# Performance work log

Measured on AMD Instinct MI355X. Metric: run time of the kernel, lower is better.

The kernel has to match this reference:

```python
import jax, jax.numpy as jnp
import numpy as np

KERNEL_SIZE = 16
STRIDE = 8
NEG = -1.0e9


def setup_inputs() -> dict:
    key = jax.random.key(0)
    k1, k2, k3, k4, k5 = jax.random.split(key, 5)
    B, C, L = 8, 512, 4096
    x = jax.random.normal(k1, (B, C, L), dtype=jnp.float32)
    mask = jax.random.randint(k2, (B, L), 0, 2).astype(bool)
    W = jax.random.normal(k3, (C, C), dtype=jnp.float32) * 0.02
    b = jax.random.normal(k4, (C,), dtype=jnp.float32) * 0.02
    v = jax.random.normal(k5, (C,), dtype=jnp.float32) * 0.02
    return {"x": x, "mask": mask, "W": W, "b": b, "v": v}


def reference(x, mask, W, b, v):
    # x: [B, C, L], mask: [B, L] (True = masked out)
    B, C, L = x.shape
    win, step = KERNEL_SIZE, STRIDE
    L_pool = 1 + (L - win) // step
    # per-token projection (identical across windows since proj is per-token)
    h = jnp.tanh(jnp.einsum('bcl,dc->bld', x, W) + b)      # [B, L, C]
    s = jnp.einsum('bld,d->bl', h, v)                       # [B, L]
    idx = jnp.arange(L_pool)[:, None] * step + jnp.arange(win)[None, :]
    sw = s[:, idx]
    mw = mask[:, idx]
    sw = jnp.where(mw, NEG, sw)
    w = jax.nn.softmax(sw, axis=-1)
    w = jnp.where(mw, 0.0, w)
    norm = jnp.clip(jnp.sum(w, axis=-1, keepdims=True), 1e-6, None)
    w = w / norm
    xw = x[:, :, idx]
    return jnp.einsum('bcpw,bpw->bcp', xw, w)               # [B, C, L_pool]
```

## Files before the change

kernel.cpp:

```cpp
#include <hip/hip_runtime.h>
#include <hip/hip_bf16.h>
#include <cmath>

#define Bsz 8
#define Csz 512
#define Lsz 4096
#define LPOOL 511
#define NEGV -1000000000.0f

typedef __attribute__((ext_vector_type(8))) short short8;
typedef __attribute__((ext_vector_type(4))) float float4v;

__device__ __forceinline__ float bf2f(short u) {
  unsigned int x = ((unsigned int)(unsigned short)u) << 16;
  return __builtin_bit_cast(float, x);
}

__device__ __forceinline__ void gl_lds16(const __hip_bfloat16* g, void* l) {
  __builtin_amdgcn_global_load_lds(
      (const __attribute__((address_space(1))) unsigned int*)g,
      (__attribute__((address_space(3))) unsigned int*)l, 16, 0, 0);
}

__global__ __launch_bounds__(256) void stage1(const float* __restrict__ x,
    __hip_bfloat16* __restrict__ xTs, __hip_bfloat16* __restrict__ xbf,
    const unsigned char* __restrict__ mb, int* __restrict__ flag,
    const float* __restrict__ W, __hip_bfloat16* __restrict__ Wts) {
  const int tid = threadIdx.x;
  const int bid = blockIdx.x;
  if (bid < 4096) {
    __shared__ float sX[64][65];
    const int lt = bid & 63, ct = (bid >> 6) & 7, b = bid >> 9;
    const int l0 = lt * 64;
    const float* xb = x + ((size_t)b * Csz + ct * 64) * Lsz + l0;
    #pragma unroll
    for (int it = 0; it < 4; ++it) {
      int c = it * 16 + (tid >> 4);
      int l = (tid & 15) * 4;
      *(float4*)(&sX[c][l]) = *(const float4*)(xb + (size_t)c * Lsz + l);
    }
    __syncthreads();
    #pragma unroll
    for (int it = 0; it < 2; ++it) {
      int u = it * 256 + tid;
      int cg = u >> 6, ll = u & 63;
      __hip_bfloat16 hb[8];
      #pragma unroll
      for (int j = 0; j < 8; ++j)
        hb[j] = __float2bfloat16(sX[cg * 8 + j][ll]);
      int m = b * Lsz + l0 + ll;
      int mt = m >> 7, row = m & 127;
      int cglob = ct * 64 + cg * 8;
      int ks = cglob >> 5, seg = (cglob >> 3) & 3;
      *(short8*)(xTs + (((size_t)mt * 16 + ks) * 512 + seg * 128 + row) * 8) = *(short8*)hb;
    }
    #pragma unroll
    for (int it = 0; it < 2; ++it) {
      int u = it * 256 + tid;
      int cg = u >> 3, lseg = u & 7;
      __hip_bfloat16 hb[8];
      #pragma unroll
      for (int j = 0; j < 8; ++j)
        hb[j] = __float2bfloat16(sX[cg][lseg * 8 + j]);
      *(short8*)(xbf + ((size_t)b * Csz + ct * 64 + cg) * Lsz + l0 + lseg * 8) = *(short8*)hb;
    }
  } else {
    const int pb = bid - 4096;
    if (pb == 0) {
      __shared__ int sf;
      if (tid == 0) sf = 0;
      __syncthreads();
      int f = 0;
      for (int i = tid; i < 4096; i += 256)
        if ((i & 3) && mb[i]) f = 1;
      if (f) atomicOr(&sf, 1);
      __syncthreads();
      if (tid == 0) *flag = sf;
    } else {
      int tg = (pb - 1) * 256 + tid;
      int d = tg >> 6, cg = tg & 63;
      float4 w0 = *(const float4*)(W + (size_t)d * 512 + cg * 8);
      float4 w1 = *(const float4*)(W + (size_t)d * 512 + cg * 8 + 4);
      __hip_bfloat16 hb[8];
      hb[0] = __float2bfloat16(w0.x); hb[1] = __float2bfloat16(w0.y);
      hb[2] = __float2bfloat16(w0.z); hb[3] = __float2bfloat16(w0.w);
      hb[4] = __float2bfloat16(w1.x); hb[5] = __float2bfloat16(w1.y);
      hb[6] = __float2bfloat16(w1.z); hb[7] = __float2bfloat16(w1.w);
      int nt = d >> 7, row = d & 127, ks = cg >> 2, seg = cg & 3;
      *(short8*)(Wts + (((size_t)nt * 16 + ks) * 512 + seg * 128 + row) * 8) = *(short8*)hb;
    }
  }
}

__global__ __launch_bounds__(512, 2) void gemm_bf16(
    const __hip_bfloat16* __restrict__ xTs, const __hip_bfloat16* __restrict__ Wts,
    const float* __restrict__ bias, const float* __restrict__ v,
    float* __restrict__ s) {
  __shared__ short8 sAv[512];
  __shared__ short8 sBv[2048];
  __shared__ float s_acc[128];
  const int tid = threadIdx.x;
  const int lane = tid & 63, wave = tid >> 6;
  const int lr = lane & 15, quad = lane >> 4;
  const int mh = wave & 1, nq = wave >> 1;
  const int mt = blockIdx.x;
  const __hip_bfloat16* aT = xTs + (size_t)mt * 65536;

  if (tid < 128) s_acc[tid] = 0.f;

  float bl[8], vl[8];
  #pragma unroll
  for (int nf = 0; nf < 8; ++nf) {
    int n = nq * 128 + nf * 16 + lr;
    bl[nf] = bias[n]; vl[nf] = v[n];
  }

  float4v acc[4][8];
  #pragma unroll
  for (int i = 0; i < 4; ++i)
    #pragma unroll
    for (int j = 0; j < 8; ++j) acc[i][j] = (float4v)0.f;

  for (int ks = 0; ks < 16; ++ks) {
    __syncthreads();
    gl_lds16(aT + (size_t)ks * 4096 + (size_t)(wave * 64 + lane) * 8,
             &sAv[wave * 64]);
    #pragma unroll
    for (int it = 0; it < 4; ++it) {
      int job = wave * 4 + it;
      int nt = job >> 3, seg = (job >> 1) & 3, half = job & 1;
      const __hip_bfloat16* gb = Wts +
          (((size_t)nt * 16 + ks) * 512 + seg * 128 + half * 64 + lane) * 8;
      gl_lds16(gb, &sBv[seg * 512 + nt * 128 + half * 64]);
    }
    __syncthreads();
    short8 af[4], bfr[8];
    #pragma unroll
    for (int mf = 0; mf < 4; ++mf)
      af[mf] = sAv[quad * 128 + mh * 64 + mf * 16 + lr];
    #pragma unroll
    for (int nf = 0; nf < 8; ++nf)
      bfr[nf] = sBv[quad * 512 + nq * 128 + nf * 16 + lr];
    #pragma unroll
    for (int mf = 0; mf < 4; ++mf)
      #pragma unroll
      for (int nf = 0; nf < 8; ++nf)
        acc[mf][nf] = __builtin_amdgcn_mfma_f32_16x16x32_bf16(af[mf], bfr[nf], acc[mf][nf], 0, 0, 0);
  }

  __syncthreads();
  #pragma unroll
  for (int mf = 0; mf < 4; ++mf) {
    #pragma unroll
    for (int reg = 0; reg < 4; ++reg) {
      float p = 0.f;
      #pragma unroll
      for (int nf = 0; nf < 8; ++nf)
        p += tanhf(acc[mf][nf][reg] + bl[nf]) * vl[nf];
      p += __shfl_xor(p, 1, 16);
      p += __shfl_xor(p, 2, 16);
      p += __shfl_xor(p, 4, 16);
      p += __shfl_xor(p, 8, 16);
      if (lr == 0)
        atomicAdd(&s_acc[mh * 64 + mf * 16 + quad * 4 + reg], p);
    }
  }
  __syncthreads();
  if (tid < 128) s[mt * 128 + tid] = s_acc[tid];
}

__global__ __launch_bounds__(256) void pool2(const __hip_bfloat16* __restrict__ xbf,
    const float* __restrict__ s, const void* __restrict__ mask,
    const int* __restrict__ flag, float* __restrict__ out) {
  __shared__ float wl[8][17];
  const int t = threadIdx.x;
  const int p0 = blockIdx.x * 8, b = blockIdx.y;
  if (t < 8 && p0 + t < LPOOL) {
    const int p = p0 + t;
    const bool u8 = (*flag != 0);
    const unsigned char* m8 = (const unsigned char*)mask;
    const int* m32 = (const int*)mask;
    const int base = b * Lsz + p * 8;
    float sv[16]; int mv[16];
    float mx = -3.4e38f;
    #pragma unroll
    for (int w = 0; w < 16; ++w) {
      int mk = u8 ? (int)m8[base + w] : m32[base + w];
      float val = mk ? NEGV : s[base + w];
      sv[w] = val; mv[w] = mk;
      mx = fmaxf(mx, val);
    }
    float sum = 0.f;
    #pragma unroll
    for (int w = 0; w < 16; ++w) { sv[w] = expf(sv[w] - mx); sum += sv[w]; }
    float inv = 1.0f / sum;
    float norm = 0.f;
    #pragma unroll
    for (int w = 0; w < 16; ++w) { sv[w] = mv[w] ? 0.f : sv[w] * inv; norm += sv[w]; }
    norm = fmaxf(norm, 1e-6f);
    float rn = 1.0f / norm;
    #pragma unroll
    for (int w = 0; w < 16; ++w) wl[t][w] = sv[w] * rn;
  }
  __syncthreads();
  const int ci = t >> 3, pi = t & 7;
  const int p = p0 + pi;
  if (p >= LPOOL) return;
  float wr[16];
  #pragma unroll
  for (int w = 0; w < 16; ++w) wr[w] = wl[pi][w];
  #pragma unroll 4
  for (int it = 0; it < 16; ++it) {
    int c = it * 32 + ci;
    const __hip_bfloat16* xp = xbf + ((size_t)b * Csz + c) * Lsz + 8 * p;
    short8 lo = *(const short8*)xp;
    short8 hi = *(const short8*)(xp + 8);
    float acc = 0.f;
    #pragma unroll
    for (int j = 0; j < 8; ++j)
      acc += bf2f(lo[j]) * wr[j] + bf2f(hi[j]) * wr[8 + j];
    out[((size_t)b * Csz + c) * LPOOL + p] = acc;
  }
}

__global__ void detect_mask(const unsigned char* __restrict__ mb, int* __restrict__ flag) {
  __shared__ int sf;
  int t = threadIdx.x;
  if (t == 0) sf = 0;
  __syncthreads();
  int f = 0;
  for (int i = t; i < 4096; i += 256)
    if ((i & 3) && mb[i]) f = 1;
  if (f) atomicOr(&sf, 1);
  __syncthreads();
  if (t == 0) *flag = sf;
}

__global__ __launch_bounds__(256) void gemm_s_f32(const float* __restrict__ x,
    const float* __restrict__ W, const float* __restrict__ bias,
    const float* __restrict__ v, float* __restrict__ s_out) {
  __shared__ float sA[32][64];
  __shared__ float sB[32][68];
  __shared__ float s_acc[64];
  const int tid = threadIdx.x;
  const int b = blockIdx.y;
  const int l0 = blockIdx.x * 64;
  if (tid < 64) s_acc[tid] = 0.0f;
  const int tx = tid & 15;
  const int ty = tid >> 4;
  const float* xb = x + ((size_t)b * Csz) * Lsz + l0;
  for (int d0 = 0; d0 < Csz; d0 += 64) {
    float acc[4][4] = {{0.f}};
    for (int c0 = 0; c0 < Csz; c0 += 32) {
      __syncthreads();
      #pragma unroll
      for (int it = 0; it < 8; ++it) {
        int idx = tid + it * 256;
        int kc = idx >> 6, ml = idx & 63;
        sA[kc][ml] = xb[(size_t)(c0 + kc) * Lsz + ml];
      }
      #pragma unroll
      for (int it = 0; it < 8; ++it) {
        int idx = tid + it * 256;
        int kc = idx & 31, dj = idx >> 5;
        sB[kc][dj] = W[(size_t)(d0 + dj) * Csz + c0 + kc];
      }
      __syncthreads();
      #pragma unroll
      for (int kc = 0; kc < 32; ++kc) {
        float4 a  = *(const float4*)(&sA[kc][tx << 2]);
        float4 w4 = *(const float4*)(&sB[kc][ty << 2]);
        acc[0][0] += a.x * w4.x; acc[0][1] += a.x * w4.y; acc[0][2] += a.x * w4.z; acc[0][3] += a.x * w4.w;
        acc[1][0] += a.y * w4.x; acc[1][1] += a.y * w4.y; acc[1][2] += a.y * w4.z; acc[1][3] += a.y * w4.w;
        acc[2][0] += a.z * w4.x; acc[2][1] += a.z * w4.y; acc[2][2] += a.z * w4.z; acc[2][3] += a.z * w4.w;
        acc[3][0] += a.w * w4.x; acc[3][1] += a.w * w4.y; acc[3][2] += a.w * w4.z; acc[3][3] += a.w * w4.w;
      }
    }
    float part[4] = {0.f, 0.f, 0.f, 0.f};
    #pragma unroll
    for (int j = 0; j < 4; ++j) {
      int d = d0 + (ty << 2) + j;
      float bj = bias[d], vj = v[d];
      #pragma unroll
      for (int i = 0; i < 4; ++i)
        part[i] += tanhf(acc[i][j] + bj) * vj;
    }
    #pragma unroll
    for (int i = 0; i < 4; ++i)
      atomicAdd(&s_acc[(tx << 2) + i], part[i]);
  }
  __syncthreads();
  if (tid < 64) s_out[(size_t)b * Lsz + l0 + tid] = s_acc[tid];
}

__global__ void win_weights(const float* __restrict__ s, const void* __restrict__ mask,
                            const int* __restrict__ flag, float* __restrict__ wgt) {
  int t = blockIdx.x * blockDim.x + threadIdx.x;
  if (t >= Bsz * LPOOL) return;
  int b = t / LPOOL, p = t - b * LPOOL;
  const bool u8 = (*flag != 0);
  const unsigned char* m8 = (const unsigned char*)mask;
  const int* m32 = (const int*)mask;
  float sv[16]; int mv[16];
  float mx = -3.4e38f;
  int base = b * Lsz + p * 8;
  #pragma unroll
  for (int w = 0; w < 16; ++w) {
    int mk = u8 ? (int)m8[base + w] : m32[base + w];
    float val = mk ? NEGV : s[base + w];
    sv[w] = val; mv[w] = mk;
    mx = fmaxf(mx, val);
  }
  float sum = 0.f;
  #pragma unroll
  for (int w = 0; w < 16; ++w) { sv[w] = expf(sv[w] - mx); sum += sv[w]; }
  float inv = 1.0f / sum;
  float norm = 0.f;
  #pragma unroll
  for (int w = 0; w < 16; ++w) { sv[w] = mv[w] ? 0.f : sv[w] * inv; norm += sv[w]; }
  norm = fmaxf(norm, 1e-6f);
  float rn = 1.0f / norm;
  #pragma unroll
  for (int w = 0; w < 16; ++w) wgt[t * 16 + w] = sv[w] * rn;
}

__global__ __launch_bounds__(256) void pool_out(const float* __restrict__ x,
    const float* __restrict__ wgt, float* __restrict__ out) {
  __shared__ float xrow[Lsz];
  int bc = blockIdx.x;
  int c = bc & (Csz - 1);
  int b = bc >> 9;
  const float* xr = x + ((size_t)b * Csz + c) * Lsz;
  int tid = threadIdx.x;
  #pragma unroll
  for (int it = 0; it < 4; ++it) {
    int idx = (tid + it * 256) << 2;
    *(float4*)(&xrow[idx]) = *(const float4*)(&xr[idx]);
  }
  __syncthreads();
  const float* wb = wgt + (size_t)b * LPOOL * 16;
  float* ob = out + ((size_t)b * Csz + c) * LPOOL;
  for (int p = tid; p < LPOOL; p += 256) {
    const float4* wp = (const float4*)(wb + p * 16);
    const float4* xp = (const float4*)(&xrow[p * 8]);
    float acc = 0.f;
    #pragma unroll
    for (int q = 0; q < 4; ++q) {
      float4 wv = wp[q], xv = xp[q];
      acc += xv.x * wv.x + xv.y * wv.y + xv.z * wv.z + xv.w * wv.w;
    }
    ob[p] = acc;
  }
}

extern "C" void kernel_launch(void* const* d_in, const int* in_sizes, int n_in,
                              void* d_out, int out_size, void* d_ws, size_t ws_size,
                              hipStream_t stream) {
  const float* x    = (const float*)d_in[0];
  const void*  mask = d_in[1];
  const float* W    = (const float*)d_in[2];
  const float* bias = (const float*)d_in[3];
  const float* v    = (const float*)d_in[4];
  float* out = (float*)d_out;

  char* wsb = (char*)d_ws;
  int*   flag = (int*)wsb;
  float* s    = (float*)(wsb + 256);
  float* wgt  = (float*)(wsb + 131328);
  __hip_bfloat16* Wts = (__hip_bfloat16*)(wsb + 393216);
  __hip_bfloat16* xTs = (__hip_bfloat16*)(wsb + 917504);
  __hip_bfloat16* xbf = (__hip_bfloat16*)(wsb + 917504 + 33554432);
  const size_t NEED = 917504 + 33554432 + 33554432;

  if (ws_size >= NEED) {
    stage1<<<4096 + 129, 256, 0, stream>>>(x, xTs, xbf,
        (const unsigned char*)mask, flag, W, Wts);
    gemm_bf16<<<256, 512, 0, stream>>>(xTs, Wts, bias, v, s);
    pool2<<<dim3(64, Bsz), 256, 0, stream>>>(xbf, s, mask, flag, out);
  } else {
    detect_mask<<<1, 256, 0, stream>>>((const unsigned char*)mask, flag);
    gemm_s_f32<<<dim3(Lsz / 64, Bsz), 256, 0, stream>>>(x, W, bias, v, s);
    win_weights<<<(Bsz * LPOOL + 255) / 256, 256, 0, stream>>>(s, mask, flag, wgt);
    pool_out<<<Bsz * Csz, 256, 0, stream>>>(x, wgt, out);
  }
}
```

Before: 169.6 us.

## Fuse x transpose/bf16 conversion into GEMM and pool directly from fp32 x

Drops the separate stage1 pass that wrote transposed bf16 xTs and row-major bf16 xbf copies of x, which are 64MB of intermediate traffic. The GEMM now loads fp32 x tiles, converts and transposes them into LDS itself, and reads W fragments straight from global memory. The pool kernel reads fp32 x directly. This trades the intermediate write and read for twice the bytes per x load in pool2, uncached W reads in the GEMM, and a smaller 64-row tile per block.

```diff
diff --git a/kernel.cpp b/kernel.cpp
--- a/kernel.cpp
+++ b/kernel.cpp
@@ -16,102 +16,54 @@
   return __builtin_bit_cast(float, x);
 }
 
-__device__ __forceinline__ void gl_lds16(const __hip_bfloat16* g, void* l) {
-  __builtin_amdgcn_global_load_lds(
-      (const __attribute__((address_space(1))) unsigned int*)g,
-      (__attribute__((address_space(3))) unsigned int*)l, 16, 0, 0);
-}
-
-__global__ __launch_bounds__(256) void stage1(const float* __restrict__ x,
-    __hip_bfloat16* __restrict__ xTs, __hip_bfloat16* __restrict__ xbf,
-    const unsigned char* __restrict__ mb, int* __restrict__ flag,
-    const float* __restrict__ W, __hip_bfloat16* __restrict__ Wts) {
-  const int tid = threadIdx.x;
-  const int bid = blockIdx.x;
-  if (bid < 4096) {
-    __shared__ float sX[64][65];
-    const int lt = bid & 63, ct = (bid >> 6) & 7, b = bid >> 9;
-    const int l0 = lt * 64;
-    const float* xb = x + ((size_t)b * Csz + ct * 64) * Lsz + l0;
-    #pragma unroll
-    for (int it = 0; it < 4; ++it) {
-      int c = it * 16 + (tid >> 4);
-      int l = (tid & 15) * 4;
-      *(float4*)(&sX[c][l]) = *(const float4*)(xb + (size_t)c * Lsz + l);
-    }
+__global__ __launch_bounds__(256) void prep(const unsigned char* __restrict__ mb,
+    int* __restrict__ flag, const float* __restrict__ W,
+    __hip_bfloat16* __restrict__ Wts) {
+  const int bid = blockIdx.x, tid = threadIdx.x;
+  if (bid == 0) {
+    __shared__ int sf;
+    if (tid == 0) sf = 0;
     __syncthreads();
-    #pragma unroll
-    for (int it = 0; it < 2; ++it) {
-      int u = it * 256 + tid;
-      int cg = u >> 6, ll = u & 63;
-      __hip_bfloat16 hb[8];
-      #pragma unroll
-      for (int j = 0; j < 8; ++j)
-        hb[j] = __float2bfloat16(sX[cg * 8 + j][ll]);
-      int m = b * Lsz + l0 + ll;
-      int mt = m >> 7, row = m & 127;
-      int cglob = ct * 64 + cg * 8;
-      int ks = cglob >> 5, seg = (cglob >> 3) & 3;
-      *(short8*)(xTs + (((size_t)mt * 16 + ks) * 512 + seg * 128 + row) * 8) = *(short8*)hb;
-    }
-    #pragma unroll
-    for (int it = 0; it < 2; ++it) {
-      int u = it * 256 + tid;
-      int cg = u >> 3, lseg = u & 7;
-      __hip_bfloat16 hb[8];
-      #pragma unroll
-      for (int j = 0; j < 8; ++j)
-        hb[j] = __float2bfloat16(sX[cg][lseg * 8 + j]);
-      *(short8*)(xbf + ((size_t)b * Csz + ct * 64 + cg) * Lsz + l0 + lseg * 8) = *(short8*)hb;
-    }
+    int f = 0;
+    for (int i = tid; i < 4096; i += 256)
+      if ((i & 3) && mb[i]) f = 1;
+    if (f) atomicOr(&sf, 1);
+    __syncthreads();
+    if (tid == 0) *flag = sf;
   } else {
-    const int pb = bid - 4096;
-    if (pb == 0) {
-      __shared__ int sf;
-      if (tid == 0) sf = 0;
-      __syncthreads();
-      int f = 0;
-      for (int i = tid; i < 4096; i += 256)
-        if ((i & 3) && mb[i]) f = 1;
-      if (f) atomicOr(&sf, 1);
-      __syncthreads();
-      if (tid == 0) *flag = sf;
-    } else {
-      int tg = (pb - 1) * 256 + tid;
-      int d = tg >> 6, cg = tg & 63;
-      float4 w0 = *(const float4*)(W + (size_t)d * 512 + cg * 8);
-      float4 w1 = *(const float4*)(W + (size_t)d * 512 + cg * 8 + 4);
-      __hip_bfloat16 hb[8];
-      hb[0] = __float2bfloat16(w0.x); hb[1] = __float2bfloat16(w0.y);
-      hb[2] = __float2bfloat16(w0.z); hb[3] = __float2bfloat16(w0.w);
-      hb[4] = __float2bfloat16(w1.x); hb[5] = __float2bfloat16(w1.y);
-      hb[6] = __float2bfloat16(w1.z); hb[7] = __float2bfloat16(w1.w);
-      int nt = d >> 7, row = d & 127, ks = cg >> 2, seg = cg & 3;
-      *(short8*)(Wts + (((size_t)nt * 16 + ks) * 512 + seg * 128 + row) * 8) = *(short8*)hb;
-    }
-  }
-}
-
-__global__ __launch_bounds__(512, 2) void gemm_bf16(
-    const __hip_bfloat16* __restrict__ xTs, const __hip_bfloat16* __restrict__ Wts,
+    int tg = (bid - 1) * 256 + tid;
+    int d = tg >> 6, cg = tg & 63;
+    float4 w0 = *(const float4*)(W + (size_t)d * 512 + cg * 8);
+    float4 w1 = *(const float4*)(W + (size_t)d * 512 + cg * 8 + 4);
+    __hip_bfloat16 hb[8];
+    hb[0] = __float2bfloat16(w0.x); hb[1] = __float2bfloat16(w0.y);
+    hb[2] = __float2bfloat16(w0.z); hb[3] = __float2bfloat16(w0.w);
+    hb[4] = __float2bfloat16(w1.x); hb[5] = __float2bfloat16(w1.y);
+    hb[6] = __float2bfloat16(w1.z); hb[7] = __float2bfloat16(w1.w);
+    int nt = d >> 7, row = d & 127, ks = cg >> 2, seg = cg & 3;
+    *(short8*)(Wts + (((size_t)nt * 16 + ks) * 512 + seg * 128 + row) * 8) = *(short8*)hb;
+  }
+}
+
+__global__ __launch_bounds__(256, 2) void gemm_fused(
+    const float* __restrict__ x, const __hip_bfloat16* __restrict__ Wts,
     const float* __restrict__ bias, const float* __restrict__ v,
     float* __restrict__ s) {
-  __shared__ short8 sAv[512];
-  __shared__ short8 sBv[2048];
-  __shared__ float s_acc[128];
+  __shared__ short8 aU[4096];
+  __shared__ float sX[32][65];
+  __shared__ float s_acc[64];
   const int tid = threadIdx.x;
   const int lane = tid & 63, wave = tid >> 6;
   const int lr = lane & 15, quad = lane >> 4;
-  const int mh = wave & 1, nq = wave >> 1;
-  const int mt = blockIdx.x;
-  const __hip_bfloat16* aT = xTs + (size_t)mt * 65536;
-
-  if (tid < 128) s_acc[tid] = 0.f;
+  const int bid = blockIdx.x;
+  const int b = bid >> 6, l0 = (bid & 63) * 64;
+
+  if (tid < 64) s_acc[tid] = 0.f;
 
   float bl[8], vl[8];
   #pragma unroll
   for (int nf = 0; nf < 8; ++nf) {
-    int n = nq * 128 + nf * 16 + lr;
+    int n = wave * 128 + nf * 16 + lr;
     bl[nf] = bias[n]; vl[nf] = v[n];
   }
 
@@ -121,26 +73,36 @@
     #pragma unroll
     for (int j = 0; j < 8; ++j) acc[i][j] = (float4v)0.f;
 
+  const float* xb = x + ((size_t)b * Csz) * Lsz + l0;
+  const int cl = tid >> 4;
+  const int l4 = (tid & 15) * 4;
+  const int cg = tid >> 6;
+  const int ll = tid & 63;
+  for (int cc = 0; cc < 16; ++cc) {
+    #pragma unroll
+    for (int it = 0; it < 2; ++it) {
+      int c = it * 16 + cl;
+      *(float4*)(&sX[c][l4]) = *(const float4*)(xb + (size_t)(cc * 32 + c) * Lsz + l4);
+    }
+    __syncthreads();
+    __hip_bfloat16 hb[8];
+    #pragma unroll
+    for (int j = 0; j < 8; ++j)
+      hb[j] = __float2bfloat16(sX[cg * 8 + j][ll]);
+    aU[cc * 256 + cg * 64 + ll] = *(short8*)hb;
+    __syncthreads();
+  }
+
+  const short8* bBase = (const short8*)Wts + (size_t)wave * 8192 + quad * 128 + lr;
   for (int ks = 0; ks < 16; ++ks) {
-    __syncthreads();
-    gl_lds16(aT + (size_t)ks * 4096 + (size_t)(wave * 64 + lane) * 8,
-             &sAv[wave * 64]);
-    #pragma unroll
-    for (int it = 0; it < 4; ++it) {
-      int job = wave * 4 + it;
-      int nt = job >> 3, seg = (job >> 1) & 3, half = job & 1;
-      const __hip_bfloat16* gb = Wts +
-          (((size_t)nt * 16 + ks) * 512 + seg * 128 + half * 64 + lane) * 8;
-      gl_lds16(gb, &sBv[seg * 512 + nt * 128 + half * 64]);
-    }
-    __syncthreads();
-    short8 af[4], bfr[8];
+    short8 af[4];
     #pragma unroll
     for (int mf = 0; mf < 4; ++mf)
-      af[mf] = sAv[quad * 128 + mh * 64 + mf * 16 + lr];
+      af[mf] = aU[ks * 256 + quad * 64 + mf * 16 + lr];
+    short8 bfr[8];
     #pragma unroll
     for (int nf = 0; nf < 8; ++nf)
-      bfr[nf] = sBv[quad * 512 + nq * 128 + nf * 16 + lr];
+      bfr[nf] = bBase[(size_t)ks * 512 + nf * 16];
     #pragma unroll
     for (int mf = 0; mf < 4; ++mf)
       #pragma unroll
@@ -162,14 +124,14 @@
       p += __shfl_xor(p, 4, 16);
       p += __shfl_xor(p, 8, 16);
       if (lr == 0)
-        atomicAdd(&s_acc[mh * 64 + mf * 16 + quad * 4 + reg], p);
-    }
-  }
-  __syncthreads();
-  if (tid < 128) s[mt * 128 + tid] = s_acc[tid];
-}
-
-__global__ __launch_bounds__(256) void pool2(const __hip_bfloat16* __restrict__ xbf,
+        atomicAdd(&s_acc[mf * 16 + quad * 4 + reg], p);
+    }
+  }
+  __syncthreads();
+  if (tid < 64) s[(size_t)bid * 64 + tid] = s_acc[tid];
+}
+
+__global__ __launch_bounds__(256) void pool2(const float* __restrict__ x,
     const float* __restrict__ s, const void* __restrict__ mask,
     const int* __restrict__ flag, float* __restrict__ out) {
   __shared__ float wl[8][17];
@@ -212,13 +174,14 @@
   #pragma unroll 4
   for (int it = 0; it < 16; ++it) {
     int c = it * 32 + ci;
-    const __hip_bfloat16* xp = xbf + ((size_t)b * Csz + c) * Lsz + 8 * p;
-    short8 lo = *(const short8*)xp;
-    short8 hi = *(const short8*)(xp + 8);
+    const float* xp = x + ((size_t)b * Csz + c) * Lsz + 8 * p;
     float acc = 0.f;
     #pragma unroll
-    for (int j = 0; j < 8; ++j)
-      acc += bf2f(lo[j]) * wr[j] + bf2f(hi[j]) * wr[8 + j];
+    for (int q = 0; q < 4; ++q) {
+      float4 xv = *(const float4*)(xp + q * 4);
+      acc += xv.x * wr[q * 4] + xv.y * wr[q * 4 + 1] +
+             xv.z * wr[q * 4 + 2] + xv.w * wr[q * 4 + 3];
+    }
     out[((size_t)b * Csz + c) * LPOOL + p] = acc;
   }
 }
@@ -365,18 +328,15 @@
 
   char* wsb = (char*)d_ws;
   int*   flag = (int*)wsb;
-  float* s    = (float*)(wsb + 256);
-  float* wgt  = (float*)(wsb + 131328);
-  __hip_bfloat16* Wts = (__hip_bfloat16*)(wsb + 393216);
-  __hip_bfloat16* xTs = (__hip_bfloat16*)(wsb + 917504);
-  __hip_bfloat16* xbf = (__hip_bfloat16*)(wsb + 917504 + 33554432);
-  const size_t NEED = 917504 + 33554432 + 33554432;
+  float* s    = (float*)(wsb + 512);
+  float* wgt  = (float*)(wsb + 131584);
+  __hip_bfloat16* Wts = (__hip_bfloat16*)(wsb + 524288);
+  const size_t NEED = 524288 + 524288;
 
   if (ws_size >= NEED) {
-    stage1<<<4096 + 129, 256, 0, stream>>>(x, xTs, xbf,
-        (const unsigned char*)mask, flag, W, Wts);
-    gemm_bf16<<<256, 512, 0, stream>>>(xTs, Wts, bias, v, s);
-    pool2<<<dim3(64, Bsz), 256, 0, stream>>>(xbf, s, mask, flag, out);
+    prep<<<129, 256, 0, stream>>>((const unsigned char*)mask, flag, W, Wts);
+    gemm_fused<<<512, 256, 0, stream>>>(x, Wts, bias, v, s);
+    pool2<<<dim3(64, Bsz), 256, 0, stream>>>(x, s, mask, flag, out);
   } else {
     detect_mask<<<1, 256, 0, stream>>>((const unsigned char*)mask, flag);
     gemm_s_f32<<<dim3(Lsz / 64, Bsz), 256, 0, stream>>>(x, W, bias, v, s);
```

Result: faster. 161.6 us (-4.7%).
